# Performance work log

Hardware: AMD Instinct MI355X
Metric: run time of the kernel (lower is better)

Reference implementation:

```python
import jax, jax.numpy as jnp
import numpy as np

B, S, D = 4, 2048, 16
N_HEAD_ARG = 16
# Faithful to source bug: effective num heads = hidden_size (D), head_size = D // n_head_arg.
# This only type-checks when head_size == 1 (D == n_head_arg), as in the repo config.
HEADS = D                     # self.n_head = hidden_size
HEAD_SIZE = D // N_HEAD_ARG   # = 1


def setup_inputs() -> dict:
    key = jax.random.key(0)
    k_x, k_wq, k_bq, k_wo, k_bo = jax.random.split(key, 5)
    x = jax.random.normal(k_x, (B, S, D), dtype=jnp.float32)
    # torch Linear init scale ~ 1/sqrt(in_features); store weights as [in, out]
    s = 1.0 / np.sqrt(D)
    w_qkv = jax.random.uniform(k_wq, (D, 3 * D), minval=-s, maxval=s, dtype=jnp.float32)
    b_qkv = jax.random.uniform(k_bq, (3 * D,), minval=-s, maxval=s, dtype=jnp.float32)
    w_out = jax.random.uniform(k_wo, (D, D), minval=-s, maxval=s, dtype=jnp.float32)
    b_out = jax.random.uniform(k_bo, (D,), minval=-s, maxval=s, dtype=jnp.float32)
    return {"x": x, "w_qkv": w_qkv, "b_qkv": b_qkv, "w_out": w_out, "b_out": b_out}


def reference(x, w_qkv, b_qkv, w_out, b_out):
    b, s, _ = x.shape
    qkv = x @ w_qkv + b_qkv                      # [b, s, 3D]
    q, k, v = jnp.split(qkv, 3, axis=-1)         # each [b, s, D]
    # [b, s, H, hs] -> [b, H, s, hs]
    q = q.reshape(b, s, HEADS, HEAD_SIZE).transpose(0, 2, 1, 3)
    k = k.reshape(b, s, HEADS, HEAD_SIZE).transpose(0, 2, 1, 3)
    v = v.reshape(b, s, HEADS, HEAD_SIZE).transpose(0, 2, 1, 3)
    scale = 1.0 / jnp.sqrt(jnp.asarray(HEAD_SIZE, dtype=x.dtype))
    scores = jnp.einsum('bhqd,bhkd->bhqk', q, k) * scale   # [b, H, s, s]
    causal = jnp.tril(jnp.ones((s, s), dtype=bool))
    scores = jnp.where(causal, scores, jnp.asarray(-jnp.inf, dtype=scores.dtype))
    attn = jax.nn.softmax(scores, axis=-1)
    # dropout is identity in eval mode (correctness baseline)
    out = jnp.einsum('bhqk,bhkd->bhqd', attn, v)            # [b, H, s, hs]
    out = out.transpose(0, 2, 1, 3).reshape(b, s, HEADS * HEAD_SIZE)
    return out @ w_out + b_out
```

## Files before the change

### kernel.cpp

```cpp
#include <hip/hip_runtime.h>
#include <math.h>

#define BB 4
#define SS 2048
#define DD 16
#define HH 16
#define NM 32

#define EXP2(x) __builtin_amdgcn_exp2f(x)
#define LOG2E 1.44269504088896340736f

__constant__ float INVFACT[NM] = {
    1.000000000e+00f, 1.000000000e+00f, 5.000000000e-01f, 1.666666667e-01f,
    4.166666667e-02f, 8.333333333e-03f, 1.388888889e-03f, 1.984126984e-04f,
    2.480158730e-05f, 2.755731922e-06f, 2.755731922e-07f, 2.505210839e-08f,
    2.087675699e-09f, 1.605904384e-10f, 1.147074560e-11f, 7.647163732e-13f,
    4.779477332e-14f, 2.811457254e-15f, 1.561920697e-16f, 8.220635247e-18f,
    4.110317623e-19f, 1.957294106e-20f, 8.896791392e-22f, 3.868170171e-23f,
    1.611737571e-24f, 6.446950284e-26f, 2.479596263e-27f, 9.183689864e-29f,
    3.279889237e-30f, 1.130996289e-31f, 3.769987629e-33f, 1.216125042e-34f};

#define UNPACK16(X4, XR)                                                   \
  const float4 x0_ = (X4)[0], x1_ = (X4)[1], x2_ = (X4)[2], x3_ = (X4)[3]; \
  const float XR[16] = {x0_.x, x0_.y, x0_.z, x0_.w, x1_.x, x1_.y, x1_.z,   \
                        x1_.w, x2_.x, x2_.y, x2_.z, x2_.w, x3_.x, x3_.y,   \
                        x3_.z, x3_.w};

__global__ __launch_bounds__(1024) void fused_attn_kernel(
    const float* __restrict__ x, const float* __restrict__ w_qkv,
    const float* __restrict__ b_qkv, float* __restrict__ AO) {
  __shared__ float kl[SS];
  __shared__ float vl[SS];
  __shared__ float ql[512];
  __shared__ float2 SP[32 * 32];
  __shared__ float PR[8 * 64];

  const int blk = blockIdx.x;
  const int sub = blk & 3;
  const int bh = blk >> 2;
  const int b = bh >> 4, h = bh & 15;
  const int t = threadIdx.x;
  const int R = (sub + 1) * 512;
  const int NB = (sub + 1) * 8;
  const int q0 = sub * 512;

  {
    float wq[16], wk[16], wv[16];
#pragma unroll
    for (int i = 0; i < 16; ++i) {
      wq[i] = w_qkv[i * 48 + h];
      wk[i] = w_qkv[i * 48 + 16 + h];
      wv[i] = w_qkv[i * 48 + 32 + h];
    }
    const float bq = b_qkv[h], bk = b_qkv[16 + h], bv = b_qkv[32 + h];
    for (int r = 0; r * 1024 < R; ++r) {
      const int j = r * 1024 + t;
      if (j < R) {
        const float4* X4 = (const float4*)(x + ((size_t)b * SS + j) * DD);
        UNPACK16(X4, xr);
        float kk = bk, vv = bv;
#pragma unroll
        for (int i = 0; i < 16; ++i) {
          kk = fmaf(xr[i], wk[i], kk);
          vv = fmaf(xr[i], wv[i], vv);
        }
        kl[j] = kk;
        vl[j] = vv;
        if ((unsigned)(j - q0) < 512u) {
          float qq = bq;
#pragma unroll
          for (int i = 0; i < 16; ++i) qq = fmaf(xr[i], wq[i], qq);
          ql[j - q0] = qq;
        }
      }
    }
  }
  __syncthreads();

  {
    const int jb = t >> 5;
    const int mg = (t >> 2) & 7;
    const int js = t & 3;
    if (jb < NB) {
      float s0 = 0.f, s1 = 0.f, s2 = 0.f, s3 = 0.f;
      float w0 = 0.f, w1 = 0.f, w2 = 0.f, w3 = 0.f;
      const float4* kp = (const float4*)(kl + jb * 64);
      const float4* vp = (const float4*)(vl + jb * 64);
#pragma unroll
      for (int u = 0; u < 4; ++u) {
        const float4 kk = kp[u * 4 + js];
        const float4 vv = vp[u * 4 + js];
        const float ke[4] = {kk.x, kk.y, kk.z, kk.w};
        const float ve[4] = {vv.x, vv.y, vv.z, vv.w};
#pragma unroll
        for (int e = 0; e < 4; ++e) {
          const float k = ke[e], v = ve[e];
          const float k2 = k * k, k4 = k2 * k2, k8 = k4 * k4, k16 = k8 * k8;
          float p = (mg & 1) ? k4 : 1.f;
          p *= (mg & 2) ? k8 : 1.f;
          p *= (mg & 4) ? k16 : 1.f;
          s0 += p; w0 = fmaf(p, v, w0);
          p *= k;
          s1 += p; w1 = fmaf(p, v, w1);
          p *= k;
          s2 += p; w2 = fmaf(p, v, w2);
          p *= k;
          s3 += p; w3 = fmaf(p, v, w3);
        }
      }
      s0 += __shfl_xor(s0, 1); s0 += __shfl_xor(s0, 2);
      s1 += __shfl_xor(s1, 1); s1 += __shfl_xor(s1, 2);
      s2 += __shfl_xor(s2, 1); s2 += __shfl_xor(s2, 2);
      s3 += __shfl_xor(s3, 1); s3 += __shfl_xor(s3, 2);
      w0 += __shfl_xor(w0, 1); w0 += __shfl_xor(w0, 2);
      w1 += __shfl_xor(w1, 1); w1 += __shfl_xor(w1, 2);
      w2 += __shfl_xor(w2, 1); w2 += __shfl_xor(w2, 2);
      w3 += __shfl_xor(w3, 1); w3 += __shfl_xor(w3, 2);
      const int m = mg * 4 + js;
      const float c = INVFACT[m];
      const float ss = (js == 0) ? s0 : (js == 1) ? s1 : (js == 2) ? s2 : s3;
      const float tt = (js == 0) ? w0 : (js == 1) ? w1 : (js == 2) ? w2 : w3;
      SP[jb * 32 + m] = make_float2(ss * c, tt * c);
    }
  }
  __syncthreads();

  if (t < 512) {
    const int l = t & 63;
    const int w = t >> 6;
    const int qb = (q0 >> 6) + w;

    {
      const float* SPf = (const float*)SP;
      float run = 0.f;
      for (int jb = 0; jb < qb; ++jb) run += SPf[jb * 64 + l];
      PR[w * 64 + l] = run;
    }

    const int i = q0 + t;
    const float q = ql[t];
    const float qs = q * LOG2E;

    float num = 0.f, den = 0.f;
    {
      const float4* bc4 = (const float4*)(PR + w * 64);
      float p = 1.f;
#pragma unroll
      for (int g = 0; g < 16; ++g) {
        const float4 st = bc4[g];
        den = fmaf(p, st.x, den);
        num = fmaf(p, st.y, num);
        p *= q;
        den = fmaf(p, st.z, den);
        num = fmaf(p, st.w, num);
        p *= q;
      }
    }

    float ld = 0.f, ad = 0.f;
    const float4* kd4 = (const float4*)(kl + qb * 64);
    const float4* vd4 = (const float4*)(vl + qb * 64);
#pragma unroll
    for (int g = 0; g < 16; ++g) {
      const float4 k4 = kd4[g], v4 = vd4[g];
      const int jj = 4 * g;
      float e;
      e = EXP2(qs * k4.x); e = (jj + 0 <= l) ? e : 0.f; ld += e; ad = fmaf(e, v4.x, ad);
      e = EXP2(qs * k4.y); e = (jj + 1 <= l) ? e : 0.f; ld += e; ad = fmaf(e, v4.y, ad);
      e = EXP2(qs * k4.z); e = (jj + 2 <= l) ? e : 0.f; ld += e; ad = fmaf(e, v4.z, ad);
      e = EXP2(qs * k4.w); e = (jj + 3 <= l) ? e : 0.f; ld += e; ad = fmaf(e, v4.w, ad);
    }

    AO[(size_t)bh * SS + i] = (ad + num) / (ld + den);
  }
}

__global__ __launch_bounds__(256) void proj_kernel(
    const float* __restrict__ AO, const float* __restrict__ w,
    const float* __restrict__ bias, float* __restrict__ out) {
  __shared__ float wct[DD * 68];
  __shared__ float aol[256];
  __shared__ float bs[DD];
  const int t = threadIdx.x;
  const int b = blockIdx.x >> 7;
  const int s_base = (blockIdx.x * 16) & (SS - 1);

  wct[(t & 15) * 68 + (t >> 4)] = w[t];
  if (t < DD) bs[t] = bias[t];
  {
    const int h = t >> 4, row_l = t & 15;
    const int bh = b * HH + h;
    aol[row_l * 16 + h] = AO[(size_t)bh * SS + s_base + row_l];
  }
  __syncthreads();

  const int row_l = t >> 4, d = t & 15;
  const float4* ao4 = (const float4*)aol;
  const float4* wc4 = (const float4*)wct;

  float y = bs[d];
#pragma unroll
  for (int g = 0; g < 4; ++g) {
    const float4 xv = ao4[row_l * 4 + g];
    const float4 wv = wc4[d * 17 + g];
    y = fmaf(xv.x, wv.x, y);
    y = fmaf(xv.y, wv.y, y);
    y = fmaf(xv.z, wv.z, y);
    y = fmaf(xv.w, wv.w, y);
  }
  out[(size_t)blockIdx.x * 256 + t] = y;
}

extern "C" void kernel_launch(void* const* d_in, const int* in_sizes, int n_in,
                              void* d_out, int out_size, void* d_ws,
                              size_t ws_size, hipStream_t stream) {
  const float* x = (const float*)d_in[0];
  const float* w_qkv = (const float*)d_in[1];
  const float* b_qkv = (const float*)d_in[2];
  const float* w_out = (const float*)d_in[3];
  const float* b_out = (const float*)d_in[4];
  float* out = (float*)d_out;

  float* AO = (float*)d_ws;

  fused_attn_kernel<<<256, 1024, 0, stream>>>(x, w_qkv, b_qkv, AO);
  proj_kernel<<<512, 256, 0, stream>>>(AO, w_out, b_out, out);
}
```

Baseline: 70.58 us.

## Fuse output projection into attention kernel via inter-block flag synchronization

Removes the separate projection kernel. Each attention block publishes its per-head results and sets a release flag. The head-0 block of each (batch, query chunk) group spin-waits on the 16 flags for that group, then computes the output projection for its 512 rows. This saves one kernel launch and the extra pass over AO, but adds a memset launch and relies on all 256 blocks being co-resident to avoid deadlock, and the spinning blocks can stall.

```diff
diff --git a/kernel.cpp b/kernel.cpp
--- a/kernel.cpp
+++ b/kernel.cpp
@@ -28,12 +28,16 @@
 
 __global__ __launch_bounds__(1024) void fused_attn_kernel(
     const float* __restrict__ x, const float* __restrict__ w_qkv,
-    const float* __restrict__ b_qkv, float* __restrict__ AO) {
+    const float* __restrict__ b_qkv, const float* __restrict__ w_out,
+    const float* __restrict__ b_out, float* __restrict__ AO,
+    unsigned* __restrict__ flags, float* __restrict__ out) {
   __shared__ float kl[SS];
   __shared__ float vl[SS];
   __shared__ float ql[512];
   __shared__ float2 SP[32 * 32];
   __shared__ float PR[8 * 64];
+  __shared__ float wo[256];
+  __shared__ float bo[16];
 
   const int blk = blockIdx.x;
   const int sub = blk & 3;
@@ -43,6 +47,7 @@
   const int R = (sub + 1) * 512;
   const int NB = (sub + 1) * 8;
   const int q0 = sub * 512;
+  const int grp = b * 4 + sub;
 
   {
     float wq[16], wk[16], wv[16];
@@ -171,44 +176,47 @@
       e = EXP2(qs * k4.w); e = (jj + 3 <= l) ? e : 0.f; ld += e; ad = fmaf(e, v4.w, ad);
     }
 
-    AO[(size_t)bh * SS + i] = (ad + num) / (ld + den);
-  }
-}
-
-__global__ __launch_bounds__(256) void proj_kernel(
-    const float* __restrict__ AO, const float* __restrict__ w,
-    const float* __restrict__ bias, float* __restrict__ out) {
-  __shared__ float wct[DD * 68];
-  __shared__ float aol[256];
-  __shared__ float bs[DD];
-  const int t = threadIdx.x;
-  const int b = blockIdx.x >> 7;
-  const int s_base = (blockIdx.x * 16) & (SS - 1);
-
-  wct[(t & 15) * 68 + (t >> 4)] = w[t];
-  if (t < DD) bs[t] = bias[t];
+    const float res = (ad + num) / (ld + den);
+    __hip_atomic_store(&AO[(size_t)bh * SS + i], res, __ATOMIC_RELAXED,
+                       __HIP_MEMORY_SCOPE_AGENT);
+  }
+  __syncthreads();
+  if (t == 0)
+    __hip_atomic_store(&flags[grp * 16 + h], 1u, __ATOMIC_RELEASE,
+                       __HIP_MEMORY_SCOPE_AGENT);
+
+  if (h != 0) return;
+
+  if (t < 256) wo[t] = w_out[t];
+  if (t < 16) bo[t] = b_out[t];
+  if (t < 16) {
+    while (__hip_atomic_load(&flags[grp * 16 + t], __ATOMIC_ACQUIRE,
+                             __HIP_MEMORY_SCOPE_AGENT) == 0u) {
+      __builtin_amdgcn_s_sleep(2);
+    }
+  }
+  __syncthreads();
+
   {
-    const int h = t >> 4, row_l = t & 15;
-    const int bh = b * HH + h;
-    aol[row_l * 16 + h] = AO[(size_t)bh * SS + s_base + row_l];
-  }
-  __syncthreads();
-
-  const int row_l = t >> 4, d = t & 15;
-  const float4* ao4 = (const float4*)aol;
-  const float4* wc4 = (const float4*)wct;
-
-  float y = bs[d];
-#pragma unroll
-  for (int g = 0; g < 4; ++g) {
-    const float4 xv = ao4[row_l * 4 + g];
-    const float4 wv = wc4[d * 17 + g];
-    y = fmaf(xv.x, wv.x, y);
-    y = fmaf(xv.y, wv.y, y);
-    y = fmaf(xv.z, wv.z, y);
-    y = fmaf(xv.w, wv.w, y);
-  }
-  out[(size_t)blockIdx.x * 256 + t] = y;
+    const int row = q0 + (t >> 1);
+    const int d0 = (t & 1) * 8;
+    float a[16];
+#pragma unroll
+    for (int hh = 0; hh < 16; ++hh)
+      a[hh] = __hip_atomic_load(&AO[(size_t)(b * 16 + hh) * SS + row],
+                                __ATOMIC_RELAXED, __HIP_MEMORY_SCOPE_AGENT);
+    float y[8];
+#pragma unroll
+    for (int d = 0; d < 8; ++d) y[d] = bo[d0 + d];
+#pragma unroll
+    for (int hh = 0; hh < 16; ++hh)
+#pragma unroll
+      for (int d = 0; d < 8; ++d)
+        y[d] = fmaf(a[hh], wo[hh * 16 + d0 + d], y[d]);
+    float4* o4 = (float4*)(out + ((size_t)b * SS + row) * DD + d0);
+    o4[0] = make_float4(y[0], y[1], y[2], y[3]);
+    o4[1] = make_float4(y[4], y[5], y[6], y[7]);
+  }
 }
 
 extern "C" void kernel_launch(void* const* d_in, const int* in_sizes, int n_in,
@@ -221,8 +229,11 @@
   const float* b_out = (const float*)d_in[4];
   float* out = (float*)d_out;
 
-  float* AO = (float*)d_ws;
-
-  fused_attn_kernel<<<256, 1024, 0, stream>>>(x, w_qkv, b_qkv, AO);
-  proj_kernel<<<512, 256, 0, stream>>>(AO, w_out, b_out, out);
+  float* ws = (float*)d_ws;
+  float* AO = ws;
+  unsigned* flags = (unsigned*)(ws + 64 * SS);
+
+  hipMemsetAsync(flags, 0, 256 * sizeof(unsigned), stream);
+  fused_attn_kernel<<<256, 1024, 0, stream>>>(x, w_qkv, b_qkv, w_out, b_out,
+                                              AO, flags, out);
 }
```

New measurement: 72.81 us. 1.03x slower.
